# Kernel optimization log

Measured on AMD Instinct MI355X. Metric: run time of the kernel, lower is better.

The kernel has to match this reference:

```python
import jax, jax.numpy as jnp
import numpy as np
from jax import lax

INPUT = 78   # 26 * 3
HID = 4
L, B = 2048, 512


def _lstm_layer(x, W_ih, W_hh, b_ih, b_hh):
    """Single unidirectional LSTM layer, PyTorch gate order (i, f, g, o).
    x: [L, B, D] -> [L, B, H]"""
    H = W_hh.shape[1]
    Bsz = x.shape[1]
    # Precompute input contribution for all timesteps: [L, B, 4H]
    xg = jnp.einsum('lbd,gd->lbg', x, W_ih) + b_ih + b_hh

    def step(carry, xg_t):
        h, c = carry
        gates = xg_t + h @ W_hh.T  # [B, 4H]
        i, f, g, o = jnp.split(gates, 4, axis=-1)
        i = jax.nn.sigmoid(i)
        f = jax.nn.sigmoid(f)
        g = jnp.tanh(g)
        o = jax.nn.sigmoid(o)
        c = f * c + i * g
        h = o * jnp.tanh(c)
        return (h, c), h

    h0 = jnp.zeros((Bsz, H), x.dtype)
    c0 = jnp.zeros((Bsz, H), x.dtype)
    _, ys = lax.scan(step, (h0, c0), xg)
    return ys  # [L, B, H]


def setup_inputs() -> dict:
    key = jax.random.key(0)
    ks = jax.random.split(key, 10)
    x = jax.random.normal(ks[0], (L, B, INPUT), dtype=jnp.float32)
    lens = jax.random.randint(ks[1], (B,), 1, L + 1)  # in [1, L]
    s = 1.0 / np.sqrt(HID)
    def u(k, shape):
        return jax.random.uniform(k, shape, jnp.float32, -s, s)
    return {
        'x': x,
        'lens': lens,
        'W_ih0': u(ks[2], (4 * HID, INPUT)),
        'W_hh0': u(ks[3], (4 * HID, HID)),
        'b_ih0': u(ks[4], (4 * HID,)),
        'b_hh0': u(ks[5], (4 * HID,)),
        'W_ih1': u(ks[6], (4 * HID, HID)),
        'W_hh1': u(ks[7], (4 * HID, HID)),
        'b_ih1': u(ks[8], (4 * HID,)),
        'b_hh1': u(ks[9], (4 * HID,)),
    }


def reference(x, lens, W_ih0, W_hh0, b_ih0, b_hh0, W_ih1, W_hh1, b_ih1, b_hh1):
    # 2-layer unidirectional LSTM over padded input. Because the LSTM is causal,
    # outputs at valid positions (t < len) equal those of the packed computation;
    # we zero out positions t >= len to match packed semantics (pad_packed form).
    y0 = _lstm_layer(x, W_ih0, W_hh0, b_ih0, b_hh0)
    y1 = _lstm_layer(y0, W_ih1, W_hh1, b_ih1, b_hh1)
    mask = (jnp.arange(x.shape[0])[:, None] < lens[None, :])[:, :, None]
    return jnp.where(mask, y1, 0.0)  # [L, B, HID]
```

## Files before the change

kernel.cpp:

```cpp
#include <hip/hip_runtime.h>


#define LSEQ  2048
#define BATCH 512
#define NIN   78
#define LOG2E 1.4426950408889634f

#define WS_BIAS_F  0
#define WS_XG_F    5120
#define XG_BYTES   ((unsigned)LSEQ * BATCH * 16u * 4u)

#define RPB  128
#define TPB1 128

typedef __attribute__((ext_vector_type(2))) float vf2;

__device__ __forceinline__ float rcp_(float x) { return __builtin_amdgcn_rcpf(x); }
__device__ __forceinline__ float ex2_(float x) { return __builtin_amdgcn_exp2f(x); }
__device__ __forceinline__ vf2 pkfma(vf2 a, vf2 b, vf2 c) {
  return __builtin_elementwise_fma(a, b, c);
}

template<int CTRL>
__device__ __forceinline__ float dppf(float x) {
  int r = __builtin_amdgcn_update_dpp(0, __builtin_bit_cast(int, x), CTRL, 0xf, 0xf, false);
  return __builtin_bit_cast(float, r);
}

__global__ __launch_bounds__(TPB1) void xg_kernel(
    const float* __restrict__ x, const float* __restrict__ Wih0,
    const float* __restrict__ bih0, const float* __restrict__ bhh0,
    const float* __restrict__ bih1, const float* __restrict__ bhh1,
    float* __restrict__ ws)
{
  __shared__ float xs[RPB * NIN];
  const int tid = threadIdx.x;
  const int r0  = blockIdx.x * RPB;

  if (blockIdx.x == 0 && tid < 16) {
    const int j = tid >> 2, g = tid & 3, row = j + 4 * g;
    const float s = (g == 2) ? 2.f * LOG2E : -LOG2E;
    ws[WS_BIAS_F + tid] = s * (bih1[row] + bhh1[row]);
  }

  const float4* gx = (const float4*)(x + (size_t)r0 * NIN);
  float4* ls = (float4*)xs;
  for (int i = tid; i < RPB * NIN / 4; i += TPB1) ls[i] = gx[i];
  __syncthreads();

  const float* xr = xs + tid * NIN;
  float acc[16];
#pragma unroll
  for (int row = 0; row < 16; ++row) acc[row] = bih0[row] + bhh0[row];
  for (int k = 0; k < NIN; ++k) {
    const float xk = xr[k];
#pragma unroll
    for (int row = 0; row < 16; ++row) acc[row] += xk * Wih0[row * NIN + k];
  }
#pragma unroll
  for (int row = 0; row < 16; ++row) {
    const float s = ((row >> 2) == 2) ? 2.f * LOG2E : -LOG2E;
    acc[row] *= s;
  }
  float* o = ws + WS_XG_F + (size_t)(r0 + tid) * 16;
#pragma unroll
  for (int j = 0; j < 4; ++j) {
    float4 v = make_float4(acc[j], acc[j + 4], acc[j + 8], acc[j + 12]);
    *(float4*)(o + j * 4) = v;
  }
}

__global__ __launch_bounds__(64) void lstm_rec(
    const float* __restrict__ wsr,
    const int* __restrict__ lens,
    const float* __restrict__ Whh0, const float* __restrict__ Whh1,
    const float* __restrict__ Wih1,
    float* __restrict__ out)
{
  const int lane  = threadIdx.x;
  const int grp   = lane >> 3;
  const int sub   = lane & 7;
  const int layer = sub >> 2;
  const int j     = sub & 3;
  const int b     = blockIdx.x * 8 + grp;

  vf2 wA01[4], wA23[4], wB01[4], wB23[4];
  const float* whh = layer ? Whh1 : Whh0;
#pragma unroll
  for (int m = 0; m < 4; ++m) {
    const float s0 = -LOG2E, s1 = -LOG2E, s2 = 2.f * LOG2E, s3 = -LOG2E;
    wA01[m] = vf2{ s0 * whh[(j + 0) * 4 + m],  s1 * whh[(j + 4) * 4 + m] };
    wA23[m] = vf2{ s2 * whh[(j + 8) * 4 + m],  s3 * whh[(j + 12) * 4 + m] };
    const float t0 = layer ? s0 * Wih1[(j + 0) * 4 + m]  : 0.f;
    const float t1 = layer ? s1 * Wih1[(j + 4) * 4 + m]  : 0.f;
    const float t2 = layer ? s2 * Wih1[(j + 8) * 4 + m]  : 0.f;
    const float t3 = layer ? s3 * Wih1[(j + 12) * 4 + m] : 0.f;
    wB01[m] = vf2{ t0, t1 };
    wB23[m] = vf2{ t2, t3 };
  }
  const int len = lens[b];

  unsigned ofs = layer ? (unsigned)(j * 16)
                       : (unsigned)(WS_XG_F * 4 + (b * 16 + j * 4) * 4);
  const unsigned stride = layer ? 0u : (unsigned)(BATCH * 16 * 4);
  const unsigned maxofs = (unsigned)(WS_XG_F * 4) + XG_BYTES - 16u;

  float* sp = out + b * 4 + j;

  float h = 0.f, c = 0.f;

  auto ld4 = [&](unsigned o) -> float4 {
    o = (o > maxofs) ? maxofs : o;
    return *(const float4*)((const char*)wsr + o);
  };

  float4 buf[8];
#pragma unroll
  for (int p = 0; p < 8; ++p) { buf[p] = ld4(ofs); ofs += stride; }

  auto step = [&](const float4 b4, int t, bool do_store) {
    float A0 = dppf<0x00>(h), A1 = dppf<0x55>(h),
          A2 = dppf<0xAA>(h), A3 = dppf<0xFF>(h);
    float B0 = dppf<0x114>(A0), B1 = dppf<0x114>(A1),
          B2 = dppf<0x114>(A2), B3 = dppf<0x114>(A3);
    vf2 Av0 = { A0, A0 }, Av1 = { A1, A1 }, Av2 = { A2, A2 }, Av3 = { A3, A3 };
    vf2 Bv0 = { B0, B0 }, Bv1 = { B1, B1 }, Bv2 = { B2, B2 }, Bv3 = { B3, B3 };

    vf2 p01 = pkfma(Av0, wA01[0], vf2{ b4.x, b4.y });
    p01 = pkfma(Av1, wA01[1], p01);
    p01 = pkfma(Bv0, wB01[0], p01);
    p01 = pkfma(Bv1, wB01[1], p01);
    vf2 q01 = Av2 * wA01[2];
    q01 = pkfma(Av3, wA01[3], q01);
    q01 = pkfma(Bv2, wB01[2], q01);
    q01 = pkfma(Bv3, wB01[3], q01);
    vf2 g01 = p01 + q01;

    vf2 p23 = pkfma(Av0, wA23[0], vf2{ b4.z, b4.w });
    p23 = pkfma(Av1, wA23[1], p23);
    p23 = pkfma(Bv0, wB23[0], p23);
    p23 = pkfma(Bv1, wB23[1], p23);
    vf2 q23 = Av2 * wA23[2];
    q23 = pkfma(Av3, wA23[3], q23);
    q23 = pkfma(Bv2, wB23[2], q23);
    q23 = pkfma(Bv3, wB23[3], q23);
    vf2 g23 = p23 + q23;

    float si = rcp_(1.f + ex2_(g01.x));
    float sf = rcp_(1.f + ex2_(g01.y));
    float tg = fmaf(-2.f, rcp_(1.f + ex2_(g23.x)), 1.f);
    float so = rcp_(1.f + ex2_(g23.y));
    c = fmaf(sf, c, si * tg);
    float tc = fmaf(-2.f, rcp_(1.f + ex2_(c * (2.f * LOG2E))), 1.f);
    h = so * tc;
    if (do_store) {
      if (layer) *sp = (t < len) ? h : 0.f;
      sp += BATCH * 4;
    }
  };

  step(buf[0], -1, false);
  if (layer) { h = 0.f; c = 0.f; }
  buf[0] = ld4(ofs); ofs += stride;

#pragma unroll 8
  for (int k = 1; k <= LSEQ; ++k) {
    step(buf[k & 7], k - 1, true);
    buf[k & 7] = ld4(ofs); ofs += stride;
  }
}

extern "C" void kernel_launch(void* const* d_in, const int* in_sizes, int n_in,
                              void* d_out, int out_size, void* d_ws, size_t ws_size,
                              hipStream_t stream) {
  const float* x    = (const float*)d_in[0];
  const int*   lens = (const int*)d_in[1];
  const float* Wih0 = (const float*)d_in[2];
  const float* Whh0 = (const float*)d_in[3];
  const float* bih0 = (const float*)d_in[4];
  const float* bhh0 = (const float*)d_in[5];
  const float* Wih1 = (const float*)d_in[6];
  const float* Whh1 = (const float*)d_in[7];
  const float* bih1 = (const float*)d_in[8];
  const float* bhh1 = (const float*)d_in[9];
  float* ws  = (float*)d_ws;
  float* out = (float*)d_out;

  xg_kernel<<<(LSEQ * BATCH) / RPB, TPB1, 0, stream>>>(
      x, Wih0, bih0, bhh0, bih1, bhh1, ws);
  lstm_rec<<<BATCH / 8, 64, 0, stream>>>(
      ws, lens, Whh0, Whh1, Wih1, out);
}
```

Measured before the change: 835.5 us.

## Split LSTM recurrence one lane per gate and exchange hidden state via swizzles

Remaps the recurrent kernel so each lane computes one gate for one hidden unit, 32 lanes per batch element covering both layers, instead of 8 lanes per batch element each computing all four gates. Every lane now does a single activation, and the gate values are gathered with DPP while the hidden state is broadcast with ds_swizzle. The aim is to shorten the serial per-step dependency chain. The trade-off is 4x more blocks, so fewer batch elements per wave, and LDS-path swizzle latency sitting on the critical path in each step.

New measurement: 772.4 us. -7.5%, faster.

```diff
diff --git a/kernel.cpp b/kernel.cpp
--- a/kernel.cpp
+++ b/kernel.cpp
@@ -13,17 +13,17 @@
 #define RPB  128
 #define TPB1 128
 
-typedef __attribute__((ext_vector_type(2))) float vf2;
-
 __device__ __forceinline__ float rcp_(float x) { return __builtin_amdgcn_rcpf(x); }
 __device__ __forceinline__ float ex2_(float x) { return __builtin_amdgcn_exp2f(x); }
-__device__ __forceinline__ vf2 pkfma(vf2 a, vf2 b, vf2 c) {
-  return __builtin_elementwise_fma(a, b, c);
-}
 
 template<int CTRL>
 __device__ __forceinline__ float dppf(float x) {
   int r = __builtin_amdgcn_update_dpp(0, __builtin_bit_cast(int, x), CTRL, 0xf, 0xf, false);
+  return __builtin_bit_cast(float, r);
+}
+template<int PAT>
+__device__ __forceinline__ float swzf(float x) {
+  int r = __builtin_amdgcn_ds_swizzle(__builtin_bit_cast(int, x), PAT);
   return __builtin_bit_cast(float, r);
 }
 
@@ -78,95 +78,87 @@
     float* __restrict__ out)
 {
   const int lane  = threadIdx.x;
-  const int grp   = lane >> 3;
-  const int sub   = lane & 7;
-  const int layer = sub >> 2;
-  const int j     = sub & 3;
-  const int b     = blockIdx.x * 8 + grp;
+  const int g     = lane & 3;
+  const int j     = (lane >> 2) & 3;
+  const int layer = (lane >> 4) & 1;
+  const int b     = blockIdx.x * 2 + (lane >> 5);
 
-  vf2 wA01[4], wA23[4], wB01[4], wB23[4];
+  const float sg = (g == 2) ? 2.f * LOG2E : -LOG2E;
+  const float ka = (g == 2) ? -4.f * LOG2E : 1.f;
+  const float kb = (g == 2) ?  2.f * LOG2E : 0.f;
+
+  const int row4 = (g * 4 + j) * 4;
   const float* whh = layer ? Whh1 : Whh0;
+  float wA[4], wB[4];
 #pragma unroll
   for (int m = 0; m < 4; ++m) {
-    const float s0 = -LOG2E, s1 = -LOG2E, s2 = 2.f * LOG2E, s3 = -LOG2E;
-    wA01[m] = vf2{ s0 * whh[(j + 0) * 4 + m],  s1 * whh[(j + 4) * 4 + m] };
-    wA23[m] = vf2{ s2 * whh[(j + 8) * 4 + m],  s3 * whh[(j + 12) * 4 + m] };
-    const float t0 = layer ? s0 * Wih1[(j + 0) * 4 + m]  : 0.f;
-    const float t1 = layer ? s1 * Wih1[(j + 4) * 4 + m]  : 0.f;
-    const float t2 = layer ? s2 * Wih1[(j + 8) * 4 + m]  : 0.f;
-    const float t3 = layer ? s3 * Wih1[(j + 12) * 4 + m] : 0.f;
-    wB01[m] = vf2{ t0, t1 };
-    wB23[m] = vf2{ t2, t3 };
+    wA[m] = sg * whh[row4 + (j ^ m)];
+    wB[m] = layer ? sg * Wih1[row4 + (j ^ m)] : 0.f;
   }
   const int len = lens[b];
 
-  unsigned ofs = layer ? (unsigned)(j * 16)
-                       : (unsigned)(WS_XG_F * 4 + (b * 16 + j * 4) * 4);
+  unsigned ofs = layer ? (unsigned)((j * 4 + g) * 4)
+                       : (unsigned)(WS_XG_F * 4 + (b * 16 + j * 4 + g) * 4);
   const unsigned stride = layer ? 0u : (unsigned)(BATCH * 16 * 4);
-  const unsigned maxofs = (unsigned)(WS_XG_F * 4) + XG_BYTES - 16u;
+  const unsigned maxofs = (unsigned)(WS_XG_F * 4) + XG_BYTES - 4u;
 
   float* sp = out + b * 4 + j;
 
-  float h = 0.f, c = 0.f;
+  float A0 = 0.f, A1 = 0.f, A2 = 0.f, A3 = 0.f;
+  float B0 = 0.f, B1 = 0.f, B2 = 0.f, B3 = 0.f;
+  float cs = 0.f;
 
-  auto ld4 = [&](unsigned o) -> float4 {
+  auto ld1 = [&](unsigned o) -> float {
     o = (o > maxofs) ? maxofs : o;
-    return *(const float4*)((const char*)wsr + o);
+    return *(const float*)((const char*)wsr + o);
   };
 
-  float4 buf[8];
+  float buf[8];
 #pragma unroll
-  for (int p = 0; p < 8; ++p) { buf[p] = ld4(ofs); ofs += stride; }
+  for (int p = 0; p < 8; ++p) { buf[p] = ld1(ofs); ofs += stride; }
 
-  auto step = [&](const float4 b4, int t, bool do_store) {
-    float A0 = dppf<0x00>(h), A1 = dppf<0x55>(h),
-          A2 = dppf<0xAA>(h), A3 = dppf<0xFF>(h);
-    float B0 = dppf<0x114>(A0), B1 = dppf<0x114>(A1),
-          B2 = dppf<0x114>(A2), B3 = dppf<0x114>(A3);
-    vf2 Av0 = { A0, A0 }, Av1 = { A1, A1 }, Av2 = { A2, A2 }, Av3 = { A3, A3 };
-    vf2 Bv0 = { B0, B0 }, Bv1 = { B1, B1 }, Bv2 = { B2, B2 }, Bv3 = { B3, B3 };
+  auto step = [&](const float base, int t, bool do_store) {
+    float p0 = fmaf(A0, wA[0], base);
+    p0 = fmaf(A1, wA[1], p0);
+    float p1 = A2 * wA[2];
+    p1 = fmaf(A3, wA[3], p1);
+    float p2 = fmaf(B0, wB[0], B1 * wB[1]);
+    float p3 = fmaf(B2, wB[2], B3 * wB[3]);
+    const float P = (p0 + p1) + (p2 + p3);
 
-    vf2 p01 = pkfma(Av0, wA01[0], vf2{ b4.x, b4.y });
-    p01 = pkfma(Av1, wA01[1], p01);
-    p01 = pkfma(Bv0, wB01[0], p01);
-    p01 = pkfma(Bv1, wB01[1], p01);
-    vf2 q01 = Av2 * wA01[2];
-    q01 = pkfma(Av3, wA01[3], q01);
-    q01 = pkfma(Bv2, wB01[2], q01);
-    q01 = pkfma(Bv3, wB01[3], q01);
-    vf2 g01 = p01 + q01;
+    const float r   = rcp_(1.f + ex2_(P));
+    const float act = fmaf(ka, r, kb);
 
-    vf2 p23 = pkfma(Av0, wA23[0], vf2{ b4.z, b4.w });
-    p23 = pkfma(Av1, wA23[1], p23);
-    p23 = pkfma(Bv0, wB23[0], p23);
-    p23 = pkfma(Bv1, wB23[1], p23);
-    vf2 q23 = Av2 * wA23[2];
-    q23 = pkfma(Av3, wA23[3], q23);
-    q23 = pkfma(Bv2, wB23[2], q23);
-    q23 = pkfma(Bv3, wB23[3], q23);
-    vf2 g23 = p23 + q23;
+    const float vi = dppf<0x00>(act), vf = dppf<0x55>(act),
+                vg = dppf<0xAA>(act), vo = dppf<0xFF>(act);
 
-    float si = rcp_(1.f + ex2_(g01.x));
-    float sf = rcp_(1.f + ex2_(g01.y));
-    float tg = fmaf(-2.f, rcp_(1.f + ex2_(g23.x)), 1.f);
-    float so = rcp_(1.f + ex2_(g23.y));
-    c = fmaf(sf, c, si * tg);
-    float tc = fmaf(-2.f, rcp_(1.f + ex2_(c * (2.f * LOG2E))), 1.f);
-    h = so * tc;
+    cs = fmaf(vf, cs, vi * vg);
+    const float tc = fmaf(-2.f, rcp_(1.f + ex2_(cs)), 1.f);
+    const float hq = vo * tc;
+
+    A0 = hq;
+    A1 = swzf<0x101F>(hq);
+    A2 = swzf<0x201F>(hq);
+    A3 = swzf<0x301F>(hq);
+    B0 = swzf<0x401F>(hq);
+    B1 = swzf<0x501F>(hq);
+    B2 = swzf<0x601F>(hq);
+    B3 = swzf<0x701F>(hq);
+
     if (do_store) {
-      if (layer) *sp = (t < len) ? h : 0.f;
+      if (layer && g == 0) *sp = (t < len) ? hq : 0.f;
       sp += BATCH * 4;
     }
   };
 
   step(buf[0], -1, false);
-  if (layer) { h = 0.f; c = 0.f; }
-  buf[0] = ld4(ofs); ofs += stride;
+  if (layer) { cs = 0.f; A0 = 0.f; A1 = 0.f; A2 = 0.f; A3 = 0.f; }
+  buf[0] = ld1(ofs); ofs += stride;
 
 #pragma unroll 8
   for (int k = 1; k <= LSEQ; ++k) {
     step(buf[k & 7], k - 1, true);
-    buf[k & 7] = ld4(ofs); ofs += stride;
+    buf[k & 7] = ld1(ofs); ofs += stride;
   }
 }
 
@@ -188,6 +180,6 @@
 
   xg_kernel<<<(LSEQ * BATCH) / RPB, TPB1, 0, stream>>>(
       x, Wih0, bih0, bhh0, bih1, bhh1, ws);
-  lstm_rec<<<BATCH / 8, 64, 0, stream>>>(
+  lstm_rec<<<BATCH / 2, 64, 0, stream>>>(
       ws, lens, Whh0, Whh1, Wih1, out);
 }
```
